# Optimization experiments

Measured on AMD Instinct MI355X. Metric: run time of the kernel, lower is better.

The kernel has to match this reference:

```python
import jax, jax.numpy as jnp
import numpy as np

EMB = 1024
HEADS = 16
HEAD_SZ = 64
INNER = 4 * EMB
EPS = 1e-5


def layer_norm(x, g, b):
    mu = jnp.mean(x, axis=-1, keepdims=True)
    var = jnp.mean(jnp.square(x - mu), axis=-1, keepdims=True)
    return (x - mu) * jax.lax.rsqrt(var + EPS) * g + b


def setup_inputs() -> dict:
    key = jax.random.key(0)
    ks = jax.random.split(key, 12)
    s = 1.0 / np.sqrt(EMB)
    si = 1.0 / np.sqrt(INNER)
    return {
        "x": jax.random.normal(ks[0], (4, 2048, EMB), dtype=jnp.float32),
        "Wq": jax.random.uniform(ks[1], (EMB, HEADS * HEAD_SZ), jnp.float32, -s, s),
        "Wk": jax.random.uniform(ks[2], (EMB, HEADS * HEAD_SZ), jnp.float32, -s, s),
        "Wv": jax.random.uniform(ks[3], (EMB, HEADS * HEAD_SZ), jnp.float32, -s, s),
        "Wo": jax.random.uniform(ks[4], (HEADS * HEAD_SZ, EMB), jnp.float32, -s, s),
        "bo": jax.random.uniform(ks[5], (EMB,), jnp.float32, -s, s),
        "g1": jnp.ones((EMB,), jnp.float32),
        "b1": jnp.zeros((EMB,), jnp.float32),
        "W1": jax.random.uniform(ks[6], (EMB, INNER), jnp.float32, -s, s),
        "bf1": jax.random.uniform(ks[7], (INNER,), jnp.float32, -s, s),
        "W2": jax.random.uniform(ks[8], (INNER, EMB), jnp.float32, -si, si),
        "bf2": jax.random.uniform(ks[9], (EMB,), jnp.float32, -si, si),
        "g2": jnp.ones((EMB,), jnp.float32),
        "b2": jnp.zeros((EMB,), jnp.float32),
    }


def reference(x, Wq, Wk, Wv, Wo, bo, g1, b1, W1, bf1, W2, bf2, g2, b2):
    bs, seq, _ = x.shape
    # QKV projections -> [b, h, s, d]
    def split_heads(t):
        return t.reshape(bs, seq, HEADS, HEAD_SZ).transpose(0, 2, 1, 3)
    q = split_heads(x @ Wq)
    k = split_heads(x @ Wk)
    v = split_heads(x @ Wv)
    # scaled dot-product attention (vanilla, no mask; pdrop=0)
    attn = jnp.einsum("bhqd,bhkd->bhqk", q, k) / np.sqrt(HEAD_SZ)
    attn = jax.nn.softmax(attn, axis=-1)
    out = jnp.einsum("bhqk,bhkd->bhqd", attn, v)
    out = out.transpose(0, 2, 1, 3).reshape(bs, seq, HEADS * HEAD_SZ)
    out = out @ Wo + bo
    # residual + post-LN
    h = layer_norm(x + out, g1, b1)
    # FFN
    ff = jax.nn.relu(h @ W1 + bf1) @ W2 + bf2
    return layer_norm(h + ff, g2, b2)
```

## Files before the change

### kernel.cpp

```cpp
#include <hip/hip_runtime.h>
#include <stdint.h>

#define DEVI __device__ __forceinline__

typedef __attribute__((ext_vector_type(8))) short bf16x8;
typedef __attribute__((ext_vector_type(4))) short bf16x4;
typedef __attribute__((ext_vector_type(4))) float f32x4;
typedef unsigned short u16;
typedef uint32_t u32;

constexpr int EMB = 1024, SEQ = 2048, NTOK = 8192;
constexpr int HEADS = 16, HD = 64, INNER = 4096;

DEVI u16 f2b(float f) {
  u32 u = __float_as_uint(f);
  return (u16)((u + 0x7FFFu + ((u >> 16) & 1u)) >> 16);
}

DEVI u32 pk2(float lo, float hi) {
  u32 r;
  asm("v_cvt_pk_bf16_f32 %0, %1, %2" : "=v"(r) : "v"(lo), "v"(hi));
  return r;
}

DEVI void gload16(const void* g, void* l) {
  __builtin_amdgcn_global_load_lds(
      (const __attribute__((address_space(1))) void*)g,
      (__attribute__((address_space(3))) void*)l, 16, 0, 0);
}

DEVI int xcd_swz(int bid, int nwg) { return (bid & 7) * (nwg >> 3) + (bid >> 3); }

__global__ __launch_bounds__(256) void k_cvt(const float* __restrict__ src,
                                             u16* __restrict__ dst, int n4) {
  int i = blockIdx.x * 256 + threadIdx.x;
  if (i >= n4) return;
  float4 v = ((const float4*)src)[i];
  ushort4 o = {f2b(v.x), f2b(v.y), f2b(v.z), f2b(v.w)};
  ((ushort4*)dst)[i] = o;
}

__global__ __launch_bounds__(256) void k_cvtT(const float* __restrict__ src,
                                              u16* __restrict__ dst, int K, int N) {
  __shared__ float t[32][33];
  int bk = blockIdx.x % (K >> 5), bn = blockIdx.x / (K >> 5);
  int tx = threadIdx.x & 31, ty = threadIdx.x >> 5;
#pragma unroll
  for (int i = 0; i < 4; i++)
    t[ty + i * 8][tx] = src[(size_t)(bk * 32 + ty + i * 8) * N + bn * 32 + tx];
  __syncthreads();
#pragma unroll
  for (int i = 0; i < 4; i++)
    dst[(size_t)(bn * 32 + ty + i * 8) * K + bk * 32 + tx] = f2b(t[tx][ty + i * 8]);
}

template <int EPI>
__global__ __launch_bounds__(256, 2) void k_gemm(
    const u16* __restrict__ A, const u16* __restrict__ BT, int M, int N, int K,
    u16* __restrict__ ob0, u16* __restrict__ ob1, u16* __restrict__ ob2,
    float* __restrict__ of0, const float* __restrict__ bias,
    const float* __restrict__ res) {
  __shared__ u16 As[128 * 64];
  __shared__ u16 Bs[128 * 64];
  const int tid = threadIdx.x;
  const int lane = tid & 63, w = tid >> 6;
  const int wr = w >> 1, wc = w & 1;
  const int g = lane >> 4, c = lane & 15;
  const int nbx = N >> 7;
  const int bid = xcd_swz(blockIdx.x, gridDim.x);
  const int by = bid / nbx, bx = bid % nbx;
  const int row0 = by << 7, col0 = bx << 7;

  const f32x4 z4 = {0.f, 0.f, 0.f, 0.f};
  f32x4 acc[4][4];
#pragma unroll
  for (int m = 0; m < 4; m++)
#pragma unroll
    for (int n = 0; n < 4; n++) acc[m][n] = z4;

  for (int k0 = 0; k0 < K; k0 += 64) {
    __syncthreads();
#pragma unroll
    for (int i = 0; i < 4; i++) {
      int s = tid + (i << 8);
      int r = s >> 3, cb = s & 7;
      gload16(A + (size_t)(row0 + r) * K + (k0 + ((cb ^ (r & 7)) << 3)),
              (char*)As + s * 16);
    }
#pragma unroll
    for (int i = 0; i < 4; i++) {
      int s = tid + (i << 8);
      int r = s >> 3, cb = s & 7;
      gload16(BT + (size_t)(col0 + r) * K + (k0 + ((cb ^ (r & 7)) << 3)),
              (char*)Bs + s * 16);
    }
    __syncthreads();
#pragma unroll
    for (int kk = 0; kk < 2; kk++) {
      bf16x8 af[4], bfr[4];
#pragma unroll
      for (int m = 0; m < 4; m++) {
        int r = wr * 64 + m * 16 + c;
        int off = (r * 128 + kk * 64 + g * 16) ^ ((r & 7) << 4);
        af[m] = *(const bf16x8*)((const char*)As + off);
      }
#pragma unroll
      for (int n = 0; n < 4; n++) {
        int r = wc * 64 + n * 16 + c;
        int off = (r * 128 + kk * 64 + g * 16) ^ ((r & 7) << 4);
        bfr[n] = *(const bf16x8*)((const char*)Bs + off);
      }
#pragma unroll
      for (int m = 0; m < 4; m++)
#pragma unroll
        for (int n = 0; n < 4; n++)
          acc[m][n] =
              __builtin_amdgcn_mfma_f32_16x16x32_bf16(af[m], bfr[n], acc[m][n], 0, 0, 0);
    }
  }

#pragma unroll
  for (int m = 0; m < 4; m++) {
#pragma unroll
    for (int n = 0; n < 4; n++) {
      int ocol = col0 + wc * 64 + n * 16 + c;
      int orow_base = row0 + wr * 64 + m * 16 + 4 * g;
      if constexpr (EPI == 0) {
        int which = ocol >> 10, rem = ocol & 1023;
        int h = rem >> 6, d = rem & 63;
#pragma unroll
        for (int r = 0; r < 4; r++) {
          int orow = orow_base + r;
          int b = orow >> 11, s = orow & 2047;
          int bh = b * HEADS + h;
          float av = acc[m][n][r];
          if (which == 0)
            ob0[((size_t)bh * SEQ + s) * HD + d] = f2b(av * 0.125f);
          else if (which == 1)
            ob1[((size_t)bh * SEQ + s) * HD + d] = f2b(av);
          else
            ob2[((size_t)bh * HD + d) * SEQ + s] = f2b(av);
        }
      } else if constexpr (EPI == 1) {
        float bia = bias[ocol];
#pragma unroll
        for (int r = 0; r < 4; r++) {
          int orow = orow_base + r;
          of0[(size_t)orow * N + ocol] =
              acc[m][n][r] + bia + res[(size_t)orow * N + ocol];
        }
      } else if constexpr (EPI == 2) {
        float bia = bias[ocol];
#pragma unroll
        for (int r = 0; r < 4; r++) {
          int orow = orow_base + r;
          float v = acc[m][n][r] + bia;
          ob0[(size_t)orow * N + ocol] = f2b(v > 0.f ? v : 0.f);
        }
      } else {
        float bia = bias[ocol];
#pragma unroll
        for (int r = 0; r < 4; r++) {
          int orow = orow_base + r;
          of0[(size_t)orow * N + ocol] = acc[m][n][r] + bia;
        }
      }
    }
  }
}

__global__ __launch_bounds__(256, 2) void k_attn(const u16* __restrict__ q,
                                                 const u16* __restrict__ kb,
                                                 const u16* __restrict__ vT,
                                                 u16* __restrict__ attn) {
  __shared__ u16 Ks[2][64 * 64];
  __shared__ u16 Vs[2][64 * 64];
  const int tid = threadIdx.x, lane = tid & 63, w = tid >> 6;
  const int g = lane >> 4, c = lane & 15;
  const int blk = xcd_swz(blockIdx.x, gridDim.x);
  const int bh = blk >> 5, qb = blk & 31;
  const int b = bh >> 4, h = bh & 15;
  const u16* qh = q + (size_t)bh * SEQ * HD;
  const u16* kh = kb + (size_t)bh * SEQ * HD;
  const u16* vh = vT + (size_t)bh * HD * SEQ;
  const int qr = qb * 64 + w * 16 + c;
  bf16x8 qf0 = *(const bf16x8*)(qh + (size_t)qr * HD + 8 * g);
  bf16x8 qf1 = *(const bf16x8*)(qh + (size_t)qr * HD + 32 + 8 * g);

  const f32x4 z4 = {0.f, 0.f, 0.f, 0.f};
  f32x4 O[4];
#pragma unroll
  for (int m = 0; m < 4; m++) O[m] = z4;
  float mI = -3.0e38f, lI = 0.f;

  auto stage = [&](int kt, int buf) {
    const int kv0 = kt * 64;
#pragma unroll
    for (int i = 0; i < 2; i++) {
      int s = tid + (i << 8);
      int r = s >> 3, cb = s & 7;
      gload16(kh + (size_t)(kv0 + r) * HD + ((cb ^ (r & 7)) << 3),
              (char*)Ks[buf] + s * 16);
    }
#pragma unroll
    for (int i = 0; i < 2; i++) {
      int s = tid + (i << 8);
      int r = s >> 3, cb = s & 7;
      gload16(vh + (size_t)r * SEQ + kv0 + ((cb ^ (r & 7)) << 3),
              (char*)Vs[buf] + s * 16);
    }
  };

  stage(0, 0);
  __syncthreads();
  int cur = 0;
  constexpr int NT = SEQ / 64;
  for (int kt = 0; kt < NT; kt++) {
    if (kt + 1 < NT) stage(kt + 1, cur ^ 1);

    const char* ksb = (const char*)Ks[cur];
    f32x4 sc[4];
    __builtin_amdgcn_s_setprio(1);
#pragma unroll
    for (int m = 0; m < 4; m++) {
      int r = 16 * m + c;
      int sw = (r & 7) << 4;
      bf16x8 kf0 = *(const bf16x8*)(ksb + ((r * 128 + g * 16) ^ sw));
      bf16x8 kf1 = *(const bf16x8*)(ksb + ((r * 128 + 64 + g * 16) ^ sw));
      f32x4 a = z4;
      a = __builtin_amdgcn_mfma_f32_16x16x32_bf16(kf0, qf0, a, 0, 0, 0);
      a = __builtin_amdgcn_mfma_f32_16x16x32_bf16(kf1, qf1, a, 0, 0, 0);
      sc[m] = a;
    }
    __builtin_amdgcn_s_setprio(0);

    float mx = sc[0][0];
#pragma unroll
    for (int m = 0; m < 4; m++)
#pragma unroll
      for (int r = 0; r < 4; r++) mx = fmaxf(mx, sc[m][r]);
    mx = fmaxf(mx, __shfl_xor(mx, 16));
    mx = fmaxf(mx, __shfl_xor(mx, 32));
    float mNew = fmaxf(mI, mx);
    float alpha = __expf(mI - mNew);
    mI = mNew;
    float p[4][4];
    float rs = 0.f;
#pragma unroll
    for (int m = 0; m < 4; m++)
#pragma unroll
      for (int r = 0; r < 4; r++) {
        p[m][r] = __expf(sc[m][r] - mNew);
        rs += p[m][r];
      }
    rs += __shfl_xor(rs, 16);
    rs += __shfl_xor(rs, 32);
    lI = lI * alpha + rs;
#pragma unroll
    for (int m = 0; m < 4; m++)
#pragma unroll
      for (int r = 0; r < 4; r++) O[m][r] *= alpha;

    union V8w { bf16x8 v; u32 w4[4]; };
    V8w pa0, pa1;
    pa0.w4[0] = pk2(p[0][0], p[0][1]); pa0.w4[1] = pk2(p[0][2], p[0][3]);
    pa0.w4[2] = pk2(p[1][0], p[1][1]); pa0.w4[3] = pk2(p[1][2], p[1][3]);
    pa1.w4[0] = pk2(p[2][0], p[2][1]); pa1.w4[1] = pk2(p[2][2], p[2][3]);
    pa1.w4[2] = pk2(p[3][0], p[3][1]); pa1.w4[3] = pk2(p[3][2], p[3][3]);

    const char* vsb = (const char*)Vs[cur];
    union V8h { bf16x8 v; bf16x4 h2[2]; };
    __builtin_amdgcn_s_setprio(1);
#pragma unroll
    for (int m = 0; m < 4; m++) {
      int d = 16 * m + c;
      int s7 = d & 7;
      int rb = d * 128 + 8 * (g & 1);
      int ch = g >> 1;
      V8h v0, v1;
      v0.h2[0] = *(const bf16x4*)(vsb + rb + (((ch    ) ^ s7) << 4));
      v0.h2[1] = *(const bf16x4*)(vsb + rb + (((ch + 2) ^ s7) << 4));
      v1.h2[0] = *(const bf16x4*)(vsb + rb + (((ch + 4) ^ s7) << 4));
      v1.h2[1] = *(const bf16x4*)(vsb + rb + (((ch + 6) ^ s7) << 4));
      O[m] = __builtin_amdgcn_mfma_f32_16x16x32_bf16(v0.v, pa0.v, O[m], 0, 0, 0);
      O[m] = __builtin_amdgcn_mfma_f32_16x16x32_bf16(v1.v, pa1.v, O[m], 0, 0, 0);
    }
    __builtin_amdgcn_s_setprio(0);

    __syncthreads();
    cur ^= 1;
  }

  float inv = 1.f / lI;
#pragma unroll
  for (int m = 0; m < 4; m++) {
    ushort4 ov = {f2b(O[m][0] * inv), f2b(O[m][1] * inv),
                  f2b(O[m][2] * inv), f2b(O[m][3] * inv)};
    int col = h * 64 + 16 * m + 4 * g;
    *(ushort4*)(attn + ((size_t)(b * SEQ + qr)) * EMB + col) = ov;
  }
}

__global__ __launch_bounds__(256) void k_ln1(const float* __restrict__ y,
                                             const float* __restrict__ gw,
                                             const float* __restrict__ bw,
                                             float* __restrict__ hf,
                                             u16* __restrict__ hb) {
  const int row = blockIdx.x, tid = threadIdx.x, lane = tid & 63, w = tid >> 6;
  const float4 v = ((const float4*)(y + (size_t)row * EMB))[tid];
  float s = v.x + v.y + v.z + v.w;
  float s2 = v.x * v.x + v.y * v.y + v.z * v.z + v.w * v.w;
#pragma unroll
  for (int m = 1; m < 64; m <<= 1) {
    s += __shfl_xor(s, m);
    s2 += __shfl_xor(s2, m);
  }
  __shared__ float rs_[4], rq_[4];
  if (lane == 0) { rs_[w] = s; rq_[w] = s2; }
  __syncthreads();
  s = rs_[0] + rs_[1] + rs_[2] + rs_[3];
  s2 = rq_[0] + rq_[1] + rq_[2] + rq_[3];
  const float mu = s * (1.f / EMB);
  const float var = s2 * (1.f / EMB) - mu * mu;
  const float rstd = rsqrtf(var + 1e-5f);
  const float4 gg = ((const float4*)gw)[tid];
  const float4 bb = ((const float4*)bw)[tid];
  float4 o;
  o.x = (v.x - mu) * rstd * gg.x + bb.x;
  o.y = (v.y - mu) * rstd * gg.y + bb.y;
  o.z = (v.z - mu) * rstd * gg.z + bb.z;
  o.w = (v.w - mu) * rstd * gg.w + bb.w;
  ((float4*)(hf + (size_t)row * EMB))[tid] = o;
  ushort4 ob = {f2b(o.x), f2b(o.y), f2b(o.z), f2b(o.w)};
  ((ushort4*)(hb + (size_t)row * EMB))[tid] = ob;
}

__global__ __launch_bounds__(256) void k_ln2(const float* __restrict__ hf,
                                             const float* __restrict__ z,
                                             const float* __restrict__ gw,
                                             const float* __restrict__ bw,
                                             float* __restrict__ outp) {
  const int row = blockIdx.x, tid = threadIdx.x, lane = tid & 63, w = tid >> 6;
  float4 v = ((const float4*)(hf + (size_t)row * EMB))[tid];
  const float4 zz = ((const float4*)(z + (size_t)row * EMB))[tid];
  v.x += zz.x; v.y += zz.y; v.z += zz.z; v.w += zz.w;
  float s = v.x + v.y + v.z + v.w;
  float s2 = v.x * v.x + v.y * v.y + v.z * v.z + v.w * v.w;
#pragma unroll
  for (int m = 1; m < 64; m <<= 1) {
    s += __shfl_xor(s, m);
    s2 += __shfl_xor(s2, m);
  }
  __shared__ float rs_[4], rq_[4];
  if (lane == 0) { rs_[w] = s; rq_[w] = s2; }
  __syncthreads();
  s = rs_[0] + rs_[1] + rs_[2] + rs_[3];
  s2 = rq_[0] + rq_[1] + rq_[2] + rq_[3];
  const float mu = s * (1.f / EMB);
  const float var = s2 * (1.f / EMB) - mu * mu;
  const float rstd = rsqrtf(var + 1e-5f);
  const float4 gg = ((const float4*)gw)[tid];
  const float4 bb = ((const float4*)bw)[tid];
  float4 o;
  o.x = (v.x - mu) * rstd * gg.x + bb.x;
  o.y = (v.y - mu) * rstd * gg.y + bb.y;
  o.z = (v.z - mu) * rstd * gg.z + bb.z;
  o.w = (v.w - mu) * rstd * gg.w + bb.w;
  ((float4*)(outp + (size_t)row * EMB))[tid] = o;
}

extern "C" void kernel_launch(void* const* d_in, const int* in_sizes, int n_in,
                              void* d_out, int out_size, void* d_ws, size_t ws_size,
                              hipStream_t stream) {
  const float* x = (const float*)d_in[0];
  const float* Wq = (const float*)d_in[1];
  const float* Wk = (const float*)d_in[2];
  const float* Wv = (const float*)d_in[3];
  const float* Wo = (const float*)d_in[4];
  const float* bo = (const float*)d_in[5];
  const float* g1 = (const float*)d_in[6];
  const float* b1 = (const float*)d_in[7];
  const float* W1 = (const float*)d_in[8];
  const float* bf1 = (const float*)d_in[9];
  const float* W2 = (const float*)d_in[10];
  const float* bf2 = (const float*)d_in[11];
  const float* g2 = (const float*)d_in[12];
  const float* b2 = (const float*)d_in[13];
  float* out = (float*)d_out;

  char* ws = (char*)d_ws;
  size_t off = 0;
  auto alloc = [&](size_t bytes) {
    char* p = ws + off;
    off += (bytes + 255) & ~(size_t)255;
    return p;
  };
  u16* xb = (u16*)alloc((size_t)NTOK * EMB * 2);
  u16* wqkvT = (u16*)alloc((size_t)3072 * 1024 * 2);
  u16* qB = (u16*)alloc((size_t)NTOK * EMB * 2);
  u16* kB = (u16*)alloc((size_t)NTOK * EMB * 2);
  u16* vTB = (u16*)alloc((size_t)NTOK * EMB * 2);
  u16* woT = (u16*)alloc((size_t)1024 * 1024 * 2);
  u16* w1T = (u16*)alloc((size_t)4096 * 1024 * 2);
  u16* w2T = (u16*)alloc((size_t)1024 * 4096 * 2);
  float* y = (float*)alloc((size_t)NTOK * EMB * 4);
  u16* ff1 = (u16*)alloc((size_t)NTOK * INNER * 2);
  u16* attn = xb;
  float* hf = (float*)qB;
  u16* hb = vTB;
  float* z = y;

  k_cvt<<<NTOK * EMB / 4 / 256, 256, 0, stream>>>(x, xb, NTOK * EMB / 4);
  k_cvtT<<<1024, 256, 0, stream>>>(Wq, wqkvT, 1024, 1024);
  k_cvtT<<<1024, 256, 0, stream>>>(Wk, wqkvT + 1048576, 1024, 1024);
  k_cvtT<<<1024, 256, 0, stream>>>(Wv, wqkvT + 2097152, 1024, 1024);
  k_cvtT<<<1024, 256, 0, stream>>>(Wo, woT, 1024, 1024);
  k_cvtT<<<4096, 256, 0, stream>>>(W1, w1T, 1024, 4096);
  k_cvtT<<<4096, 256, 0, stream>>>(W2, w2T, 4096, 1024);
  k_gemm<0><<<(NTOK / 128) * (3072 / 128), 256, 0, stream>>>(
      xb, wqkvT, NTOK, 3072, 1024, qB, kB, vTB, nullptr, nullptr, nullptr);
  k_attn<<<64 * 32, 256, 0, stream>>>(qB, kB, vTB, attn);
  k_gemm<1><<<(NTOK / 128) * (1024 / 128), 256, 0, stream>>>(
      attn, woT, NTOK, 1024, 1024, nullptr, nullptr, nullptr, y, bo, x);
  k_ln1<<<NTOK, 256, 0, stream>>>(y, g1, b1, hf, hb);
  k_gemm<2><<<(NTOK / 128) * (4096 / 128), 256, 0, stream>>>(
      hb, w1T, NTOK, 4096, 1024, ff1, nullptr, nullptr, nullptr, bf1, nullptr);
  k_gemm<3><<<(NTOK / 128) * (1024 / 128), 256, 0, stream>>>(
      ff1, w2T, NTOK, 1024, 4096, nullptr, nullptr, nullptr, z, bf2, nullptr);
  k_ln2<<<NTOK, 256, 0, stream>>>(hf, z, g2, b2, out);
}
```

Measured before the change: 576.5 us.

## Triple-buffer GEMM with 256x128 tiles and exp2 lazy-rescale softmax in attention

The GEMM moves to 512-thread blocks computing 256x128 tiles. It uses a three-stage LDS ring with global_load_lds prefetch two tiles ahead, plus a vmcnt wait, one barrier per k-step and a raised wave priority around the MFMAs. This is meant to hide global-load latency and cut synchronisation. Attention folds log2(e) into the Q scale so it can use a raw v_exp_f32, and it skips the O/l rescale unless the row max grows by more than 8. Attention occupancy is also raised to 4 blocks per CU. Risks include LDS pressure (144KB per block) limiting residency, and small numeric drift from the lazy rescale.

```diff
diff --git a/kernel.cpp b/kernel.cpp
--- a/kernel.cpp
+++ b/kernel.cpp
@@ -20,6 +20,12 @@
 DEVI u32 pk2(float lo, float hi) {
   u32 r;
   asm("v_cvt_pk_bf16_f32 %0, %1, %2" : "=v"(r) : "v"(lo), "v"(hi));
+  return r;
+}
+
+DEVI float exp2v(float x) {
+  float r;
+  asm("v_exp_f32 %0, %1" : "=v"(r) : "v"(x));
   return r;
 }
 
@@ -55,13 +61,12 @@
 }
 
 template <int EPI>
-__global__ __launch_bounds__(256, 2) void k_gemm(
+__global__ __launch_bounds__(512, 2) void k_gemm3(
     const u16* __restrict__ A, const u16* __restrict__ BT, int M, int N, int K,
     u16* __restrict__ ob0, u16* __restrict__ ob1, u16* __restrict__ ob2,
     float* __restrict__ of0, const float* __restrict__ bias,
     const float* __restrict__ res) {
-  __shared__ u16 As[128 * 64];
-  __shared__ u16 Bs[128 * 64];
+  __shared__ u16 LDS[3][24576];
   const int tid = threadIdx.x;
   const int lane = tid & 63, w = tid >> 6;
   const int wr = w >> 1, wc = w & 1;
@@ -69,7 +74,8 @@
   const int nbx = N >> 7;
   const int bid = xcd_swz(blockIdx.x, gridDim.x);
   const int by = bid / nbx, bx = bid % nbx;
-  const int row0 = by << 7, col0 = bx << 7;
+  const int row0 = by << 8, col0 = bx << 7;
+  const int NK = K >> 6;
 
   const f32x4 z4 = {0.f, 0.f, 0.f, 0.f};
   f32x4 acc[4][4];
@@ -78,23 +84,39 @@
 #pragma unroll
     for (int n = 0; n < 4; n++) acc[m][n] = z4;
 
-  for (int k0 = 0; k0 < K; k0 += 64) {
-    __syncthreads();
+  auto stage = [&](int t, int buf) {
+    const int k0 = t << 6;
+    char* base = (char*)&LDS[buf][0];
 #pragma unroll
     for (int i = 0; i < 4; i++) {
-      int s = tid + (i << 8);
+      int s = tid + (i << 9);
       int r = s >> 3, cb = s & 7;
       gload16(A + (size_t)(row0 + r) * K + (k0 + ((cb ^ (r & 7)) << 3)),
-              (char*)As + s * 16);
-    }
-#pragma unroll
-    for (int i = 0; i < 4; i++) {
-      int s = tid + (i << 8);
+              base + s * 16);
+    }
+#pragma unroll
+    for (int i = 0; i < 2; i++) {
+      int s = tid + (i << 9);
       int r = s >> 3, cb = s & 7;
       gload16(BT + (size_t)(col0 + r) * K + (k0 + ((cb ^ (r & 7)) << 3)),
-              (char*)Bs + s * 16);
-    }
-    __syncthreads();
+              base + 32768 + s * 16);
+    }
+  };
+
+  stage(0, 0);
+  stage(1, 1);
+  for (int t = 0; t < NK; t++) {
+    __builtin_amdgcn_sched_barrier(0);
+    if (t + 1 < NK)
+      asm volatile("s_waitcnt vmcnt(6)" ::: "memory");
+    else
+      asm volatile("s_waitcnt vmcnt(0)" ::: "memory");
+    __builtin_amdgcn_s_barrier();
+    __builtin_amdgcn_sched_barrier(0);
+    if (t + 2 < NK) stage(t + 2, (t + 2) % 3);
+    const char* Ab = (const char*)&LDS[t % 3][0];
+    const char* Bb = Ab + 32768;
+    __builtin_amdgcn_s_setprio(1);
 #pragma unroll
     for (int kk = 0; kk < 2; kk++) {
       bf16x8 af[4], bfr[4];
@@ -102,13 +124,13 @@
       for (int m = 0; m < 4; m++) {
         int r = wr * 64 + m * 16 + c;
         int off = (r * 128 + kk * 64 + g * 16) ^ ((r & 7) << 4);
-        af[m] = *(const bf16x8*)((const char*)As + off);
+        af[m] = *(const bf16x8*)(Ab + off);
       }
 #pragma unroll
       for (int n = 0; n < 4; n++) {
         int r = wc * 64 + n * 16 + c;
         int off = (r * 128 + kk * 64 + g * 16) ^ ((r & 7) << 4);
-        bfr[n] = *(const bf16x8*)((const char*)Bs + off);
+        bfr[n] = *(const bf16x8*)(Bb + off);
       }
 #pragma unroll
       for (int m = 0; m < 4; m++)
@@ -117,6 +139,7 @@
           acc[m][n] =
               __builtin_amdgcn_mfma_f32_16x16x32_bf16(af[m], bfr[n], acc[m][n], 0, 0, 0);
     }
+    __builtin_amdgcn_s_setprio(0);
   }
 
 #pragma unroll
@@ -135,7 +158,7 @@
           int bh = b * HEADS + h;
           float av = acc[m][n][r];
           if (which == 0)
-            ob0[((size_t)bh * SEQ + s) * HD + d] = f2b(av * 0.125f);
+            ob0[((size_t)bh * SEQ + s) * HD + d] = f2b(av * 0.1803368801111244f);
           else if (which == 1)
             ob1[((size_t)bh * SEQ + s) * HD + d] = f2b(av);
           else
@@ -169,7 +192,7 @@
   }
 }
 
-__global__ __launch_bounds__(256, 2) void k_attn(const u16* __restrict__ q,
+__global__ __launch_bounds__(256, 4) void k_attn(const u16* __restrict__ q,
                                                  const u16* __restrict__ kb,
                                                  const u16* __restrict__ vT,
                                                  u16* __restrict__ attn) {
@@ -241,25 +264,28 @@
       for (int r = 0; r < 4; r++) mx = fmaxf(mx, sc[m][r]);
     mx = fmaxf(mx, __shfl_xor(mx, 16));
     mx = fmaxf(mx, __shfl_xor(mx, 32));
-    float mNew = fmaxf(mI, mx);
-    float alpha = __expf(mI - mNew);
-    mI = mNew;
+    if (!__all(mx - mI <= 8.f)) {
+      float mNew = fmaxf(mI, mx);
+      float alpha = exp2v(mI - mNew);
+      lI *= alpha;
+#pragma unroll
+      for (int m = 0; m < 4; m++)
+#pragma unroll
+        for (int r = 0; r < 4; r++) O[m][r] *= alpha;
+      mI = mNew;
+    }
     float p[4][4];
     float rs = 0.f;
 #pragma unroll
     for (int m = 0; m < 4; m++)
 #pragma unroll
       for (int r = 0; r < 4; r++) {
-        p[m][r] = __expf(sc[m][r] - mNew);
+        p[m][r] = exp2v(sc[m][r] - mI);
         rs += p[m][r];
       }
     rs += __shfl_xor(rs, 16);
     rs += __shfl_xor(rs, 32);
-    lI = lI * alpha + rs;
-#pragma unroll
-    for (int m = 0; m < 4; m++)
-#pragma unroll
-      for (int r = 0; r < 4; r++) O[m][r] *= alpha;
+    lI += rs;
 
     union V8w { bf16x8 v; u32 w4[4]; };
     V8w pa0, pa1;
@@ -417,15 +443,15 @@
   k_cvtT<<<1024, 256, 0, stream>>>(Wo, woT, 1024, 1024);
   k_cvtT<<<4096, 256, 0, stream>>>(W1, w1T, 1024, 4096);
   k_cvtT<<<4096, 256, 0, stream>>>(W2, w2T, 4096, 1024);
-  k_gemm<0><<<(NTOK / 128) * (3072 / 128), 256, 0, stream>>>(
+  k_gemm3<0><<<(NTOK / 256) * (3072 / 128), 512, 0, stream>>>(
       xb, wqkvT, NTOK, 3072, 1024, qB, kB, vTB, nullptr, nullptr, nullptr);
   k_attn<<<64 * 32, 256, 0, stream>>>(qB, kB, vTB, attn);
-  k_gemm<1><<<(NTOK / 128) * (1024 / 128), 256, 0, stream>>>(
+  k_gemm3<1><<<(NTOK / 256) * (1024 / 128), 512, 0, stream>>>(
       attn, woT, NTOK, 1024, 1024, nullptr, nullptr, nullptr, y, bo, x);
   k_ln1<<<NTOK, 256, 0, stream>>>(y, g1, b1, hf, hb);
-  k_gemm<2><<<(NTOK / 128) * (4096 / 128), 256, 0, stream>>>(
+  k_gemm3<2><<<(NTOK / 256) * (4096 / 128), 512, 0, stream>>>(
       hb, w1T, NTOK, 4096, 1024, ff1, nullptr, nullptr, nullptr, bf1, nullptr);
-  k_gemm<3><<<(NTOK / 128) * (1024 / 128), 256, 0, stream>>>(
+  k_gemm3<3><<<(NTOK / 256) * (1024 / 128), 512, 0, stream>>>(
       ff1, w2T, NTOK, 1024, 4096, nullptr, nullptr, nullptr, z, bf2, nullptr);
   k_ln2<<<NTOK, 256, 0, stream>>>(hf, z, g2, b2, out);
 }
```

Result: no change. 574.1 us (-0.4%).
